# Performance work log

Hardware: AMD Instinct MI355X
Metric: run time of the kernel (lower is better)

Reference implementation:

```python
import jax, jax.numpy as jnp
import numpy as np

N_RULES = 64  # R
OUT_PER_RULE = 64  # O, fc out = R*O = 4096


def setup_inputs() -> dict:
    key = jax.random.key(0)
    k1, k2, k3, k4 = jax.random.split(key, 4)
    S, D_IN = 8192, 1024
    RO = N_RULES * OUT_PER_RULE
    X = jax.random.normal(k1, (S, D_IN), dtype=jnp.float32)
    # torch.nn.Linear-style weight [out, in] and bias [out]
    W = jax.random.normal(k2, (RO, D_IN), dtype=jnp.float32) * (1.0 / np.sqrt(D_IN))
    b = jax.random.normal(k3, (RO,), dtype=jnp.float32) * 0.01
    # rule firing strengths (computed under no_grad in the original)
    lambdas = jax.random.uniform(k4, (S, N_RULES), dtype=jnp.float32)
    return {"X": X, "W": W, "b": b, "lambdas": lambdas}


def reference(X, W, b, lambdas):
    # fc + sigmoid: [S, R*O]
    H = jax.nn.sigmoid(X @ W.T + b)
    S = H.shape[0]
    # apply_rule_strength: block-diagonal lambda_eye @ H^T is exactly a
    # rule-weighted sum over the R consecutive O-sized blocks of H.
    Hr = H.reshape(S, N_RULES, OUT_PER_RULE)  # [S, R, O]
    Y = jnp.einsum("sr,sro->so", lambdas, Hr)  # [S, O]
    return Y
```

## Files before the change

kernel.cpp:

```cpp
#include <hip/hip_runtime.h>

#define S_DIM 8192
#define K_DIM 1024
#define RO_DIM 4096
#define O_DIM 64
#define SO (S_DIM * O_DIM)
#define NSLICE 16

typedef __attribute__((ext_vector_type(8))) __bf16 bf16x8;
typedef __attribute__((ext_vector_type(4))) float floatx4;
typedef __attribute__((ext_vector_type(4))) unsigned short ushx4;
typedef __attribute__((ext_vector_type(8))) unsigned short ushx8;

__device__ inline unsigned short f2bf(float f) {
  unsigned u = __builtin_bit_cast(unsigned, f);
  u += 0x7fff + ((u >> 16) & 1);
  return (unsigned short)(u >> 16);
}
__device__ inline float bf2f(unsigned short h) {
  unsigned u = ((unsigned)h) << 16;
  return __builtin_bit_cast(float, u);
}

__global__ __launch_bounds__(256) void cast_kernel(const float* __restrict__ X,
                                                   const float* __restrict__ W,
                                                   unsigned short* __restrict__ Xb,
                                                   unsigned short* __restrict__ Wb) {
  const int NX4 = (S_DIM * K_DIM) / 4;
#pragma unroll
  for (int i = 0; i < 4; ++i) {
    int g = blockIdx.x * 1024 + i * 256 + threadIdx.x;
    float4 v;
    unsigned short* dst;
    if (g < NX4) {
      v = ((const float4*)X)[g];
      dst = Xb + (size_t)g * 4;
    } else {
      int j = g - NX4;
      v = ((const float4*)W)[j];
      dst = Wb + (size_t)j * 4;
    }
    ushx4 o;
    o.x = f2bf(v.x); o.y = f2bf(v.y); o.z = f2bf(v.z); o.w = f2bf(v.w);
    *(ushx4*)dst = o;
  }
}


template <int MB, int NB>
__device__ __forceinline__ void mfmaq(floatx4 (&acc)[8][4], const bf16x8 (&afr)[4][2],
                                      const bf16x8 (&bfr)[4][2]) {
  __builtin_amdgcn_s_setprio(1);
#pragma unroll
  for (int ks = 0; ks < 2; ++ks)
#pragma unroll
    for (int m = 0; m < 4; ++m)
#pragma unroll
      for (int n = 0; n < 2; ++n)
        acc[MB + m][NB + n] = __builtin_amdgcn_mfma_f32_16x16x32_bf16(
            afr[m][ks], bfr[NB + n][ks], acc[MB + m][NB + n], 0, 0, 0);
  __builtin_amdgcn_s_setprio(0);
}

#define BAR() __builtin_amdgcn_s_barrier()

__global__ __launch_bounds__(512, 2) void gemm_kernel(const unsigned short* __restrict__ Xb,
                                                      const unsigned short* __restrict__ Wb,
                                                      const float* __restrict__ bias,
                                                      const float* __restrict__ lam,
                                                      unsigned short* __restrict__ partial) {
  __shared__ __align__(16) unsigned char smem[135168];
  unsigned short* sm = (unsigned short*)smem;
  float* lamsh = (float*)(smem + 131072);

  const int t = threadIdx.x;
  const int lane = t & 63;
  const int w = t >> 6;
  const int wm = w >> 2;
  const int wn = w & 3;
  const int quad = lane >> 4;
  const int l16 = lane & 15;

  int id = blockIdx.y * 16 + blockIdx.x;
  int x = id & 7;
  int j = id >> 3;
  const int bx = 2 * x + (j & 1);
  const int by = j >> 1;
  const int gm0 = by * 256;
  const int gn0 = bx * 256;

  const int rowt = t >> 3;
  const int gcc = (t & 7) ^ (rowt & 7);
  const size_t goff = (size_t)rowt * K_DIM + (size_t)gcc * 8;
  const unsigned short* Abase = Xb + (size_t)gm0 * K_DIM;
  const unsigned short* Bbase = Wb + (size_t)gn0 * K_DIM;

  auto STAGE = [&](const unsigned short* gbase, int half, int ktile, int slotOff) {
#pragma unroll
    for (int jj = 0; jj < 2; ++jj) {
      const unsigned short* src =
          gbase + (size_t)(half * 128 + jj * 64) * K_DIM + ktile * 64 + goff;
      __builtin_amdgcn_global_load_lds(
          (const __attribute__((address_space(1))) void*)src,
          (__attribute__((address_space(3))) void*)(sm + slotOff + jj * 4096 + t * 8),
          16, 0, 0);
    }
  };

  STAGE(Abase, 0, 0, 0);
  STAGE(Abase, 1, 0, 8192);
  STAGE(Bbase, 0, 0, 16384);
  STAGE(Bbase, 1, 0, 24576);
  STAGE(Bbase, 0, 1, 32768 + 16384);
  STAGE(Bbase, 1, 1, 32768 + 24576);
  STAGE(Abase, 0, 1, 32768 + 0);

  {
    int i = t;
    lamsh[i] = lam[(size_t)(gm0 + (i >> 2)) * 64 + bx * 4 + (i & 3)];
    i = t + 512;
    lamsh[i] = lam[(size_t)(gm0 + (i >> 2)) * 64 + bx * 4 + (i & 3)];
  }
  asm volatile("s_waitcnt vmcnt(6)" ::: "memory");
  BAR();

  floatx4 acc[8][4];
#pragma unroll
  for (int ni = 0; ni < 4; ++ni) {
    float bv = bias[gn0 + wn * 64 + ni * 16 + l16];
#pragma unroll
    for (int mi = 0; mi < 8; ++mi) acc[mi][ni] = (floatx4){bv, bv, bv, bv};
  }

  const int cA0 = ((quad) ^ (l16 & 7)) * 8;
  const int cA1 = ((4 + quad) ^ (l16 & 7)) * 8;

  for (int kt = 0; kt < 16; ++kt) {
    const int b = kt & 1;
    const unsigned short* As = sm + b * 32768 + wm * 8192 + l16 * 64;
    const unsigned short* Bs = sm + b * 32768 + 16384 + wn * 4096 + l16 * 64;
    const int bufN = (b ^ 1) * 32768;
    const int bufC = b * 32768;

    bf16x8 afr[4][2], bfr[4][2];

#pragma unroll
    for (int m = 0; m < 4; ++m) {
      afr[m][0] = *(const bf16x8*)(As + m * 1024 + cA0);
      afr[m][1] = *(const bf16x8*)(As + m * 1024 + cA1);
    }
#pragma unroll
    for (int n = 0; n < 2; ++n) {
      bfr[n][0] = *(const bf16x8*)(Bs + n * 1024 + cA0);
      bfr[n][1] = *(const bf16x8*)(Bs + n * 1024 + cA1);
    }
    if (kt < 15) STAGE(Abase, 1, kt + 1, bufN + 8192);
    BAR();
    mfmaq<0, 0>(acc, afr, bfr);
    BAR();

#pragma unroll
    for (int n = 2; n < 4; ++n) {
      bfr[n][0] = *(const bf16x8*)(Bs + n * 1024 + cA0);
      bfr[n][1] = *(const bf16x8*)(Bs + n * 1024 + cA1);
    }
    BAR();
    mfmaq<0, 2>(acc, afr, bfr);
    BAR();

#pragma unroll
    for (int m = 0; m < 4; ++m) {
      afr[m][0] = *(const bf16x8*)(As + (4 + m) * 1024 + cA0);
      afr[m][1] = *(const bf16x8*)(As + (4 + m) * 1024 + cA1);
    }
    if (kt < 14) STAGE(Bbase, 0, kt + 2, bufC + 16384);
    BAR();
    mfmaq<4, 0>(acc, afr, bfr);
    BAR();

    if (kt < 14) {
      STAGE(Bbase, 1, kt + 2, bufC + 24576);
      STAGE(Abase, 0, kt + 2, bufC + 0);
    }
    mfmaq<4, 2>(acc, afr, bfr);
    if (kt < 14) {
      asm volatile("s_waitcnt vmcnt(6)" ::: "memory");
    } else if (kt == 14) {
      asm volatile("s_waitcnt vmcnt(0)" ::: "memory");
    }
    BAR();
  }

  __syncthreads();
  {
    unsigned short* yreg = sm + wn * 16384;
#pragma unroll
    for (int mi = 0; mi < 8; ++mi) {
#pragma unroll
      for (int r = 0; r < 4; ++r) {
        int row = wm * 128 + mi * 16 + quad * 4 + r;
        float lamv = lamsh[row * 4 + wn];
#pragma unroll
        for (int ni = 0; ni < 4; ++ni) {
          float sg = 1.f / (1.f + __expf(-acc[mi][ni][r]));
          yreg[row * 64 + ((ni ^ quad) * 16) + l16] = f2bf(lamv * sg);
        }
      }
    }
  }
  __syncthreads();
  {
    unsigned short* pb = partial + (size_t)bx * SO + (size_t)gm0 * 64;
#pragma unroll
    for (int g = 0; g < 4; ++g) {
      int idx = g * 4096 + t * 8;
      int row = idx >> 6;
      int c = idx & 63;
      int phys = row * 64 + ((((c >> 4) ^ ((row >> 2) & 3))) << 4) + (c & 15);
      float s[8];
#pragma unroll
      for (int jj = 0; jj < 8; ++jj) s[jj] = 0.f;
#pragma unroll
      for (int q = 0; q < 4; ++q) {
        ushx8 v = *(const ushx8*)(sm + q * 16384 + phys);
#pragma unroll
        for (int jj = 0; jj < 8; ++jj) s[jj] += bf2f(v[jj]);
      }
      ushx8 o;
#pragma unroll
      for (int jj = 0; jj < 8; ++jj) o[jj] = f2bf(s[jj]);
      *(ushx8*)(pb + idx) = o;
    }
  }
}

__global__ __launch_bounds__(256) void reduce_kernel(const unsigned short* __restrict__ partial,
                                                     float* __restrict__ Y) {
  int i4 = blockIdx.x * 256 + threadIdx.x;
  float s0 = 0.f, s1 = 0.f, s2 = 0.f, s3 = 0.f;
#pragma unroll
  for (int c = 0; c < NSLICE; ++c) {
    ushx4 v = ((const ushx4*)(partial + (size_t)c * SO))[i4];
    s0 += bf2f(v.x); s1 += bf2f(v.y); s2 += bf2f(v.z); s3 += bf2f(v.w);
  }
  ((float4*)Y)[i4] = (float4){s0, s1, s2, s3};
}

extern "C" void kernel_launch(void* const* d_in, const int* in_sizes, int n_in,
                              void* d_out, int out_size, void* d_ws, size_t ws_size,
                              hipStream_t stream) {
  const float* X = (const float*)d_in[0];
  const float* W = (const float*)d_in[1];
  const float* b = (const float*)d_in[2];
  const float* lam = (const float*)d_in[3];
  float* Y = (float*)d_out;

  unsigned short* Xb = (unsigned short*)d_ws;
  unsigned short* Wb = Xb + (size_t)S_DIM * K_DIM;
  unsigned short* partial = Wb + (size_t)RO_DIM * K_DIM;

  int nCast = ((S_DIM + RO_DIM) * K_DIM / 4) / 1024;
  cast_kernel<<<nCast, 256, 0, stream>>>(X, W, Xb, Wb);

  dim3 g(RO_DIM / 256, S_DIM / 256);
  gemm_kernel<<<g, 512, 0, stream>>>(Xb, Wb, b, lam, partial);

  reduce_kernel<<<SO / 1024, 256, 0, stream>>>(partial, Y);
}
```

Measured before the change: 168.6 us.

## Restructure GEMM main loop with one barrier per k-tile and inline-asm LDS reads

Replaces the four-phase per-k-tile loop, which had many block barriers, with a two-phase tile. All fragments are read with inline-asm ds_read_b128 using immediate offsets, and a single barrier per k-tile follows a full vmcnt(0) wait. The next tile's A fragments are prefetched while the second MFMA half runs, and all four global-to-LDS stages are issued together two tiles ahead. The bias and lambda loads are also hoisted before the staging. This cuts barrier and synchronisation overhead, but the vmcnt(0) wait drops the finer-grained load overlap and may expose global latency.

```diff
diff --git a/kernel.cpp b/kernel.cpp
--- a/kernel.cpp
+++ b/kernel.cpp
@@ -11,6 +11,7 @@
 typedef __attribute__((ext_vector_type(4))) float floatx4;
 typedef __attribute__((ext_vector_type(4))) unsigned short ushx4;
 typedef __attribute__((ext_vector_type(8))) unsigned short ushx8;
+typedef __attribute__((address_space(3))) const unsigned short* ldsp;
 
 __device__ inline unsigned short f2bf(float f) {
   unsigned u = __builtin_bit_cast(unsigned, f);
@@ -46,23 +47,42 @@
   }
 }
 
-
-template <int MB, int NB>
-__device__ __forceinline__ void mfmaq(floatx4 (&acc)[8][4], const bf16x8 (&afr)[4][2],
-                                      const bf16x8 (&bfr)[4][2]) {
+__device__ __forceinline__ void rd4lo(bf16x8& f0, bf16x8& f1, bf16x8& f2, bf16x8& f3, ldsp b) {
+  asm volatile("ds_read_b128 %0, %4 offset:0\n\t"
+               "ds_read_b128 %1, %4 offset:2048\n\t"
+               "ds_read_b128 %2, %4 offset:4096\n\t"
+               "ds_read_b128 %3, %4 offset:6144"
+               : "=&v"(f0), "=&v"(f1), "=&v"(f2), "=&v"(f3) : "v"(b) : "memory");
+}
+__device__ __forceinline__ void rd4hi(bf16x8& f0, bf16x8& f1, bf16x8& f2, bf16x8& f3, ldsp b) {
+  asm volatile("ds_read_b128 %0, %4 offset:8192\n\t"
+               "ds_read_b128 %1, %4 offset:10240\n\t"
+               "ds_read_b128 %2, %4 offset:12288\n\t"
+               "ds_read_b128 %3, %4 offset:14336"
+               : "=&v"(f0), "=&v"(f1), "=&v"(f2), "=&v"(f3) : "v"(b) : "memory");
+}
+
+#define LGKM0() { asm volatile("s_waitcnt lgkmcnt(0)" ::: "memory"); __builtin_amdgcn_sched_barrier(0); }
+#define LGKM8() { asm volatile("s_waitcnt lgkmcnt(8)" ::: "memory"); __builtin_amdgcn_sched_barrier(0); }
+#define VMCNT0() { asm volatile("s_waitcnt vmcnt(0)" ::: "memory"); }
+#define SB0() __builtin_amdgcn_sched_barrier(0)
+#define BAR() __builtin_amdgcn_s_barrier()
+
+template <int MB>
+__device__ __forceinline__ void mf32(floatx4 (&acc)[8][4], const bf16x8 (&af)[4][2],
+                                     const bf16x8 (&bf)[4][2]) {
   __builtin_amdgcn_s_setprio(1);
 #pragma unroll
   for (int ks = 0; ks < 2; ++ks)
 #pragma unroll
     for (int m = 0; m < 4; ++m)
 #pragma unroll
-      for (int n = 0; n < 2; ++n)
-        acc[MB + m][NB + n] = __builtin_amdgcn_mfma_f32_16x16x32_bf16(
-            afr[m][ks], bfr[NB + n][ks], acc[MB + m][NB + n], 0, 0, 0);
+      for (int n = 0; n < 4; ++n)
+        acc[MB + m][n] = __builtin_amdgcn_mfma_f32_16x16x32_bf16(
+            af[m][ks], bf[n][ks], acc[MB + m][n], 0, 0, 0);
   __builtin_amdgcn_s_setprio(0);
 }
 
-#define BAR() __builtin_amdgcn_s_barrier()
 
 __global__ __launch_bounds__(512, 2) void gemm_kernel(const unsigned short* __restrict__ Xb,
                                                       const unsigned short* __restrict__ Wb,
@@ -72,6 +92,7 @@
   __shared__ __align__(16) unsigned char smem[135168];
   unsigned short* sm = (unsigned short*)smem;
   float* lamsh = (float*)(smem + 131072);
+  auto lds3 = (__attribute__((address_space(3))) unsigned short*)smem;
 
   const int t = threadIdx.x;
   const int lane = t & 63;
@@ -107,88 +128,80 @@
     }
   };
 
+  float bv[4];
+#pragma unroll
+  for (int ni = 0; ni < 4; ++ni) bv[ni] = bias[gn0 + wn * 64 + ni * 16 + l16];
+  float lv0 = lam[(size_t)(gm0 + (t >> 2)) * 64 + bx * 4 + (t & 3)];
+  int i2 = t + 512;
+  float lv1 = lam[(size_t)(gm0 + (i2 >> 2)) * 64 + bx * 4 + (i2 & 3)];
+
   STAGE(Abase, 0, 0, 0);
   STAGE(Abase, 1, 0, 8192);
   STAGE(Bbase, 0, 0, 16384);
   STAGE(Bbase, 1, 0, 24576);
+  STAGE(Abase, 0, 1, 32768 + 0);
+  STAGE(Abase, 1, 1, 32768 + 8192);
   STAGE(Bbase, 0, 1, 32768 + 16384);
   STAGE(Bbase, 1, 1, 32768 + 24576);
-  STAGE(Abase, 0, 1, 32768 + 0);
-
-  {
-    int i = t;
-    lamsh[i] = lam[(size_t)(gm0 + (i >> 2)) * 64 + bx * 4 + (i & 3)];
-    i = t + 512;
-    lamsh[i] = lam[(size_t)(gm0 + (i >> 2)) * 64 + bx * 4 + (i & 3)];
-  }
-  asm volatile("s_waitcnt vmcnt(6)" ::: "memory");
+  lamsh[t] = lv0;
+  lamsh[t + 512] = lv1;
+  VMCNT0();
+  LGKM0();
   BAR();
 
   floatx4 acc[8][4];
 #pragma unroll
-  for (int ni = 0; ni < 4; ++ni) {
-    float bv = bias[gn0 + wn * 64 + ni * 16 + l16];
-#pragma unroll
-    for (int mi = 0; mi < 8; ++mi) acc[mi][ni] = (floatx4){bv, bv, bv, bv};
-  }
+  for (int ni = 0; ni < 4; ++ni)
+#pragma unroll
+    for (int mi = 0; mi < 8; ++mi) acc[mi][ni] = (floatx4){bv[ni], bv[ni], bv[ni], bv[ni]};
 
   const int cA0 = ((quad) ^ (l16 & 7)) * 8;
   const int cA1 = ((4 + quad) ^ (l16 & 7)) * 8;
 
-  for (int kt = 0; kt < 16; ++kt) {
-    const int b = kt & 1;
-    const unsigned short* As = sm + b * 32768 + wm * 8192 + l16 * 64;
-    const unsigned short* Bs = sm + b * 32768 + 16384 + wn * 4096 + l16 * 64;
-    const int bufN = (b ^ 1) * 32768;
-    const int bufC = b * 32768;
-
-    bf16x8 afr[4][2], bfr[4][2];
-
-#pragma unroll
-    for (int m = 0; m < 4; ++m) {
-      afr[m][0] = *(const bf16x8*)(As + m * 1024 + cA0);
-      afr[m][1] = *(const bf16x8*)(As + m * 1024 + cA1);
-    }
-#pragma unroll
-    for (int n = 0; n < 2; ++n) {
-      bfr[n][0] = *(const bf16x8*)(Bs + n * 1024 + cA0);
-      bfr[n][1] = *(const bf16x8*)(Bs + n * 1024 + cA1);
-    }
-    if (kt < 15) STAGE(Abase, 1, kt + 1, bufN + 8192);
-    BAR();
-    mfmaq<0, 0>(acc, afr, bfr);
-    BAR();
-
-#pragma unroll
-    for (int n = 2; n < 4; ++n) {
-      bfr[n][0] = *(const bf16x8*)(Bs + n * 1024 + cA0);
-      bfr[n][1] = *(const bf16x8*)(Bs + n * 1024 + cA1);
-    }
-    BAR();
-    mfmaq<0, 2>(acc, afr, bfr);
-    BAR();
-
-#pragma unroll
-    for (int m = 0; m < 4; ++m) {
-      afr[m][0] = *(const bf16x8*)(As + (4 + m) * 1024 + cA0);
-      afr[m][1] = *(const bf16x8*)(As + (4 + m) * 1024 + cA1);
-    }
-    if (kt < 14) STAGE(Bbase, 0, kt + 2, bufC + 16384);
-    BAR();
-    mfmaq<4, 0>(acc, afr, bfr);
-    BAR();
-
-    if (kt < 14) {
-      STAGE(Bbase, 1, kt + 2, bufC + 24576);
-      STAGE(Abase, 0, kt + 2, bufC + 0);
-    }
-    mfmaq<4, 2>(acc, afr, bfr);
-    if (kt < 14) {
-      asm volatile("s_waitcnt vmcnt(6)" ::: "memory");
-    } else if (kt == 14) {
-      asm volatile("s_waitcnt vmcnt(0)" ::: "memory");
-    }
-    BAR();
+  const int aoff = wm * 8192 + l16 * 64;
+  const int boff = 16384 + wn * 4096 + l16 * 64;
+  ldsp A00 = lds3 + aoff + cA0;
+  ldsp A01 = lds3 + aoff + cA1;
+  ldsp B00 = lds3 + boff + cA0;
+  ldsp B01 = lds3 + boff + cA1;
+  ldsp A10 = A00 + 32768;
+  ldsp A11 = A01 + 32768;
+  ldsp B10 = B00 + 32768;
+  ldsp B11 = B01 + 32768;
+
+  bf16x8 af0[4][2], af1[4][2], bfr[4][2];
+
+  rd4lo(af0[0][0], af0[1][0], af0[2][0], af0[3][0], A00);
+  rd4lo(af0[0][1], af0[1][1], af0[2][1], af0[3][1], A01);
+
+  auto TILE = [&](int kt, ldsp aC0, ldsp aC1, ldsp bC0, ldsp bC1,
+                  ldsp aN0, ldsp aN1, int bufC) {
+    rd4lo(bfr[0][0], bfr[1][0], bfr[2][0], bfr[3][0], bC0);
+    rd4lo(bfr[0][1], bfr[1][1], bfr[2][1], bfr[3][1], bC1);
+    rd4hi(af1[0][0], af1[1][0], af1[2][0], af1[3][0], aC0);
+    rd4hi(af1[0][1], af1[1][1], af1[2][1], af1[3][1], aC1);
+    LGKM8();
+    mf32<0>(acc, af0, bfr);
+    LGKM0();
+    if (kt < 15) {
+      VMCNT0();
+      BAR();
+      if (kt < 14) {
+        STAGE(Abase, 0, kt + 2, bufC + 0);
+        STAGE(Abase, 1, kt + 2, bufC + 8192);
+        STAGE(Bbase, 0, kt + 2, bufC + 16384);
+        STAGE(Bbase, 1, kt + 2, bufC + 24576);
+      }
+      rd4lo(af0[0][0], af0[1][0], af0[2][0], af0[3][0], aN0);
+      rd4lo(af0[0][1], af0[1][1], af0[2][1], af0[3][1], aN1);
+      SB0();
+    }
+    mf32<4>(acc, af1, bfr);
+  };
+
+  for (int k2 = 0; k2 < 16; k2 += 2) {
+    TILE(k2, A00, A01, B00, B01, A10, A11, 0);
+    TILE(k2 + 1, A10, A11, B10, B11, A00, A01, 32768);
   }
 
   __syncthreads();
```

Measured after the change: 204.3 us. +21.2%, slower.
